# Kernel optimization log

Hardware: AMD Instinct MI355X
Metric: run time of the kernel (lower is better)

The kernel has to match this reference:

```python
import jax, jax.numpy as jnp
import numpy as np
from jax.experimental.ode import odeint

B, T, NV = 2048, 256, 32   # batch, time steps, n ICU variables
H, L, OH = 64, 32, 64      # gru hidden, latent dim, ode hidden


def setup_inputs() -> dict:
    key = jax.random.key(0)
    ks = jax.random.split(key, 24)
    def rn(k, shape, s):
        return (jax.random.normal(k, shape) * s).astype(jnp.float32)
    times = jnp.broadcast_to(jnp.linspace(0.0, 48.0, T, dtype=jnp.float32), (B, T))
    values = jax.random.normal(ks[0], (B, T, NV), dtype=jnp.float32)
    mask = (jax.random.uniform(ks[1], (B, T, NV)) < 0.5).astype(jnp.float32)
    seq_lengths = jnp.sort(jax.random.randint(ks[2], (B,), 1, T + 1))[::-1]
    seq_lengths = seq_lengths.at[0].set(T).astype(jnp.int32)
    eps = jax.random.normal(ks[3], (B, L), dtype=jnp.float32)
    return {
        "times": times, "values": values, "mask": mask,
        "seq_lengths": seq_lengths, "eps": eps,
        # GRU (torch layout: gates stacked r,z,n)
        "W_ih": rn(ks[4], (3 * H, 2 * NV), 0.1), "W_hh": rn(ks[5], (3 * H, H), 0.1),
        "b_ih": rn(ks[6], (3 * H,), 0.05), "b_hh": rn(ks[7], (3 * H,), 0.05),
        # hidden -> z0 params
        "W_z0": rn(ks[8], (2 * L, H), 0.1), "b_z0": rn(ks[9], (2 * L,), 0.05),
        # ODE func MLP (small weights keep dynamics tame for dopri5)
        "ode_W1": rn(ks[10], (OH, L), 0.05), "ode_b1": rn(ks[11], (OH,), 0.02),
        "ode_W2": rn(ks[12], (OH, OH), 0.05), "ode_b2": rn(ks[13], (OH,), 0.02),
        "ode_W3": rn(ks[14], (L, OH), 0.05), "ode_b3": rn(ks[15], (L,), 0.02),
        # decoder
        "dec_W1": rn(ks[16], (H, L), 0.1), "dec_b1": rn(ks[17], (H,), 0.05),
        "dec_W2": rn(ks[18], (1, H), 0.1), "dec_b2": rn(ks[19], (1,), 0.05),
    }


def _latent_ode_fwd(times, values, mask, seq_lengths, eps,
                    W_ih, W_hh, b_ih, b_hh, W_z0, b_z0,
                    ode_W1, ode_b1, ode_W2, ode_b2, ode_W3, ode_b3,
                    dec_W1, dec_b1, dec_W2, dec_b2):
    Bx, Tx = values.shape[0], values.shape[1]
    # encoder: concat (values, mask), flip time, run GRU over first seq_len steps
    x = jnp.concatenate([values, mask], axis=-1)[:, ::-1, :]          # [B,T,2NV]
    xp = jnp.einsum('btf,gf->tbg', x, W_ih) + b_ih                    # [T,B,3H]

    def gru_step(h, inp):
        xpt, t = inp                                                  # xpt: [B,3H]
        hh = h @ W_hh.T + b_hh
        xr, xz, xn = jnp.split(xpt, 3, axis=-1)
        hr, hz, hn = jnp.split(hh, 3, axis=-1)
        r = jax.nn.sigmoid(xr + hr)
        zg = jax.nn.sigmoid(xz + hz)
        n = jnp.tanh(xn + r * hn)
        h_new = (1.0 - zg) * n + zg * h
        h = jnp.where((t < seq_lengths)[:, None], h_new, h)           # packed-seq freeze
        return h, None

    h0 = jnp.zeros((Bx, W_hh.shape[1]), values.dtype)
    h, _ = jax.lax.scan(gru_step, h0, (xp, jnp.arange(Tx)))

    z0p = h @ W_z0.T + b_z0                                           # [B,2L]
    Ld = z0p.shape[-1] // 2
    z0_mean, z0_logvar = z0p[:, :Ld], z0p[:, Ld:]
    z0 = z0_mean + eps * jnp.exp(0.5 * z0_logvar)                     # reparameterize

    def ode_f(z, t, p):
        W1, b1, W2, b2, W3, b3 = p
        hl = jnp.tanh(z @ W1.T + b1)
        hl = jnp.tanh(hl @ W2.T + b2)
        return hl @ W3.T + b3

    t_span = jnp.array([0.0, 48.0], dtype=jnp.float32)
    traj = odeint(ode_f, z0, t_span,
                  (ode_W1, ode_b1, ode_W2, ode_b2, ode_W3, ode_b3),
                  rtol=1e-7, atol=1e-9)                               # dopri5, torchdiffeq defaults
    z_final = traj[-1]

    logits = (jax.nn.relu(z_final @ dec_W1.T + dec_b1) @ dec_W2.T + dec_b2)[:, 0]
    kl = -0.5 * jnp.mean(1.0 + z0_logvar - z0_mean ** 2 - jnp.exp(z0_logvar))
    return logits, kl


def reference(times, values, mask, seq_lengths, eps,
              W_ih, W_hh, b_ih, b_hh, W_z0, b_z0,
              ode_W1, ode_b1, ode_W2, ode_b2, ode_W3, ode_b3,
              dec_W1, dec_b1, dec_W2, dec_b2):
    return _latent_ode_fwd(times, values, mask, seq_lengths, eps,
                           W_ih, W_hh, b_ih, b_hh, W_z0, b_z0,
                           ode_W1, ode_b1, ode_W2, ode_b2, ode_W3, ode_b3,
                           dec_W1, dec_b1, dec_W2, dec_b2)
```

## Files before the change

### kernel.cpp

```cpp
#include <hip/hip_runtime.h>

#define B_ 2048
#define T_ 256
#define NV_ 32
#define H_ 64
#define L_ 32
#define OH_ 64
#define NSTEP 16
#define DEPTH 6

typedef _Float16 f16x8 __attribute__((ext_vector_type(8)));
typedef _Float16 f16x4 __attribute__((ext_vector_type(4)));
typedef float f32x4 __attribute__((ext_vector_type(4)));

#define MFMA16(a, b, c) __builtin_amdgcn_mfma_f32_16x16x32_f16((a), (b), (c), 0, 0, 0)

__device__ __forceinline__ float rcp_(float x) { return __builtin_amdgcn_rcpf(x); }
__device__ __forceinline__ float sigm(float x) { return rcp_(1.0f + __expf(-x)); }
__device__ __forceinline__ float tanh_(float x) { return 2.0f * rcp_(1.0f + __expf(-2.0f * x)) - 1.0f; }

__device__ __forceinline__ f16x8 pack8(f32x4 a, f32x4 b) {
    f16x8 r;
    r[0] = (_Float16)a[0]; r[1] = (_Float16)a[1]; r[2] = (_Float16)a[2]; r[3] = (_Float16)a[3];
    r[4] = (_Float16)b[0]; r[5] = (_Float16)b[1]; r[6] = (_Float16)b[2]; r[7] = (_Float16)b[3];
    return r;
}

__global__ __launch_bounds__(256) void gru_kernel(
    const float* __restrict__ values, const float* __restrict__ mask,
    const int* __restrict__ seql, const float* __restrict__ eps,
    const float* __restrict__ W_ih, const float* __restrict__ W_hh,
    const float* __restrict__ b_ih, const float* __restrict__ b_hh,
    const float* __restrict__ W_z0, const float* __restrict__ b_z0,
    float* __restrict__ z0ws, float* __restrict__ parts)
{
    const int tid = threadIdx.x;
    const int w   = tid >> 6;
    const int l   = tid & 63;
    const int c   = l & 15;
    const int g4  = l >> 4;
    const int b0  = blockIdx.x * 16;

    __shared__ unsigned h_u32[2][16][36];
    __shared__ float    zp_lds[16][68];
    __shared__ float    red_lds[4];
    __shared__ unsigned cnt;

    for (int i = tid; i < 2 * 16 * 36; i += 256) (&h_u32[0][0][0])[i] = 0u;
    if (tid == 0) cnt = 0u;

    f16x8 bih[3][2], bhh[3][2];
#pragma unroll
    for (int gate = 0; gate < 3; ++gate) {
#pragma unroll
        for (int kt = 0; kt < 2; ++kt) {
            const float* p1 = W_ih + (gate * 64 + w * 16 + c) * 64 + kt * 32 + g4 * 8;
            bih[gate][kt] = pack8(*(const f32x4*)p1, *(const f32x4*)(p1 + 4));
            const float* p2 = W_hh + (gate * 64 + w * 16 + c) * 64 + kt * 32 + g4 * 8;
            bhh[gate][kt] = pack8(*(const f32x4*)p2, *(const f32x4*)(p2 + 4));
        }
    }

    f32x4 bRq, bZq, bNXq, bNHq;
#pragma unroll
    for (int r = 0; r < 4; ++r) {
        const int f = w * 16 + g4 * 4 + r;
        bRq[r]  = b_ih[f]       + b_hh[f];
        bZq[r]  = b_ih[64 + f]  + b_hh[64 + f];
        bNXq[r] = b_ih[128 + f];
        bNHq[r] = b_hh[128 + f];
    }

    const int sl_c = seql[b0 + c];
    const int tmax = seql[b0];
    float hp[4] = {0.f, 0.f, 0.f, 0.f};

    const float* vrow = values + (size_t)(b0 + c) * T_ * NV_ + g4 * 8;
    const float* mrow = mask   + (size_t)(b0 + c) * T_ * NV_ + g4 * 8;

#define DECLSET(S) f32x4 S##v0, S##v1, S##m0, S##m1
    DECLSET(A); DECLSET(B); DECLSET(C); DECLSET(D); DECLSET(E); DECLSET(F);
#define FILLSET(S, tc) do {                                                  \
        const int tt_ = ((tc) < tmax) ? (tc) : 0;                            \
        const float* vp_ = vrow + (T_ - 1 - tt_) * NV_;                      \
        const float* mp_ = mrow + (T_ - 1 - tt_) * NV_;                      \
        S##v0 = *(const f32x4*)vp_; S##v1 = *(const f32x4*)(vp_ + 4);        \
        S##m0 = *(const f32x4*)mp_; S##m1 = *(const f32x4*)(mp_ + 4);        \
    } while (0)
    FILLSET(A, 0); FILLSET(B, 1); FILLSET(C, 2);
    FILLSET(D, 3); FILLSET(E, 4); FILLSET(F, 5);

    __syncthreads();

#define GSTEP(S, tc) do {                                                    \
        f16x8 ha0 = *(const f16x8*)&h_u32[(tc) & 1][c][4 * g4];              \
        f16x8 ha1 = *(const f16x8*)&h_u32[(tc) & 1][c][16 + 4 * g4];         \
        f16x8 xa0 = pack8(S##v0, S##v1);                                     \
        f16x8 xa1 = pack8(S##m0, S##m1);                                     \
        FILLSET(S, (tc) + DEPTH);                                            \
        f32x4 accR  = MFMA16(bih[0][0], xa0, bRq);                           \
        f32x4 accNX = MFMA16(bih[2][0], xa0, bNXq);                          \
        f32x4 accZ  = MFMA16(bih[1][0], xa0, bZq);                           \
        accR  = MFMA16(bih[0][1], xa1, accR);                                \
        accNX = MFMA16(bih[2][1], xa1, accNX);                               \
        accZ  = MFMA16(bih[1][1], xa1, accZ);                                \
        f32x4 accNH = MFMA16(bhh[2][0], ha0, bNHq);                          \
        accR  = MFMA16(bhh[0][0], ha0, accR);                                \
        accNH = MFMA16(bhh[2][1], ha1, accNH);                               \
        accR  = MFMA16(bhh[0][1], ha1, accR);                                \
        accZ  = MFMA16(bhh[1][0], ha0, accZ);                                \
        accZ  = MFMA16(bhh[1][1], ha1, accZ);                                \
        const bool act = ((tc) < sl_c);                                      \
        _Pragma("unroll")                                                    \
        for (int r = 0; r < 4; ++r) {                                        \
            float rr   = sigm(accR[r]);                                      \
            float zz   = sigm(accZ[r]);                                      \
            float nn   = tanh_(accNX[r] + rr * accNH[r]);                    \
            float hnew = nn + zz * (hp[r] - nn);                             \
            if (act) hp[r] = hnew;                                           \
        }                                                                    \
        f16x4 hq;                                                            \
        _Pragma("unroll")                                                    \
        for (int r = 0; r < 4; ++r) hq[r] = (_Float16)hp[r];                 \
        *(f16x4*)&h_u32[((tc) & 1) ^ 1][c][8 * w + 2 * g4] = hq;             \
        asm volatile("s_waitcnt lgkmcnt(0)" ::: "memory");                   \
        if (l == 0) atomicAdd(&cnt, 1u);                                     \
        asm volatile("" ::: "memory");                                       \
        {                                                                    \
            const unsigned tgt_ = 4u * ((unsigned)(tc) + 1u);                \
            while (__builtin_amdgcn_readfirstlane(                           \
                       *(volatile unsigned*)&cnt) < tgt_) { }                \
        }                                                                    \
        asm volatile("" ::: "memory");                                       \
    } while (0)

    int t = 0;
    while (true) {
        GSTEP(A, t); if (++t >= tmax) break;
        GSTEP(B, t); if (++t >= tmax) break;
        GSTEP(C, t); if (++t >= tmax) break;
        GSTEP(D, t); if (++t >= tmax) break;
        GSTEP(E, t); if (++t >= tmax) break;
        GSTEP(F, t); if (++t >= tmax) break;
    }

    f16x8 az0f[2];
#pragma unroll
    for (int kt = 0; kt < 2; ++kt) {
        const float* p = W_z0 + (w * 16 + c) * 64 + kt * 32 + g4 * 8;
        az0f[kt] = pack8(*(const f32x4*)p, *(const f32x4*)(p + 4));
    }
    const int fin = tmax & 1;
    f16x8 hf0 = *(const f16x8*)&h_u32[fin][c][4 * g4];
    f16x8 hf1 = *(const f16x8*)&h_u32[fin][c][16 + 4 * g4];
    f32x4 az;
#pragma unroll
    for (int r = 0; r < 4; ++r) az[r] = b_z0[w * 16 + g4 * 4 + r];
    az = MFMA16(az0f[0], hf0, az);
    az = MFMA16(az0f[1], hf1, az);
    *(f32x4*)&zp_lds[c][w * 16 + g4 * 4] = az;
    __syncthreads();

    const int row = tid >> 4;
    const int j2  = (tid & 15) * 2;
    float m0 = zp_lds[row][j2],      m1 = zp_lds[row][j2 + 1];
    float v0 = zp_lds[row][32 + j2], v1 = zp_lds[row][32 + j2 + 1];
    const float* erow = eps + (size_t)(b0 + row) * L_;
    float e0 = erow[j2], e1 = erow[j2 + 1];
    float* zrow = z0ws + (size_t)(b0 + row) * L_;
    float s0 = __expf(0.5f * v0), s1 = __expf(0.5f * v1);
    zrow[j2]     = m0 + e0 * s0;
    zrow[j2 + 1] = m1 + e1 * s1;
    float kls = (1.0f + v0 - m0 * m0 - s0 * s0) + (1.0f + v1 - m1 * m1 - s1 * s1);
#pragma unroll
    for (int off = 32; off >= 1; off >>= 1) kls += __shfl_down(kls, off);
    if (l == 0) red_lds[w] = kls;
    __syncthreads();
    if (tid == 0) parts[blockIdx.x] = red_lds[0] + red_lds[1] + red_lds[2] + red_lds[3];
}

__global__ __launch_bounds__(64) void ode_kernel(
    const float* __restrict__ z0ws,
    const float* __restrict__ oW1, const float* __restrict__ ob1,
    const float* __restrict__ oW2, const float* __restrict__ ob2,
    const float* __restrict__ oW3, const float* __restrict__ ob3,
    const float* __restrict__ dW1, const float* __restrict__ db1,
    const float* __restrict__ dW2, const float* __restrict__ db2,
    float* __restrict__ out)
{
    const int l  = threadIdx.x;
    const int c  = l & 15;
    const int g4 = l >> 4;
    const int b0 = blockIdx.x * 16;

    __shared__ _Float16 zbuf[16][40];
    __shared__ _Float16 buf1[16][72];
    __shared__ _Float16 buf2[16][72];

    f16x8 w1f[4], d1f[4], w2f[4][2], w3f[2][2];
#pragma unroll
    for (int mt = 0; mt < 4; ++mt) {
        const float* p = oW1 + (mt * 16 + c) * 32 + g4 * 8;
        w1f[mt] = pack8(*(const f32x4*)p, *(const f32x4*)(p + 4));
        const float* q = dW1 + (mt * 16 + c) * 32 + g4 * 8;
        d1f[mt] = pack8(*(const f32x4*)q, *(const f32x4*)(q + 4));
#pragma unroll
        for (int kt = 0; kt < 2; ++kt) {
            const float* r = oW2 + (mt * 16 + c) * 64 + kt * 32 + g4 * 8;
            w2f[mt][kt] = pack8(*(const f32x4*)r, *(const f32x4*)(r + 4));
        }
    }
#pragma unroll
    for (int mt = 0; mt < 2; ++mt) {
#pragma unroll
        for (int kt = 0; kt < 2; ++kt) {
            const float* r = oW3 + (mt * 16 + c) * 64 + kt * 32 + g4 * 8;
            w3f[mt][kt] = pack8(*(const f32x4*)r, *(const f32x4*)(r + 4));
        }
    }

    f32x4 b1q[4], b2q[4], d1q[4], w2q[4], b3q[2];
#pragma unroll
    for (int mt = 0; mt < 4; ++mt) {
#pragma unroll
        for (int r = 0; r < 4; ++r) {
            b1q[mt][r] = ob1[mt * 16 + g4 * 4 + r];
            b2q[mt][r] = ob2[mt * 16 + g4 * 4 + r];
            d1q[mt][r] = db1[mt * 16 + g4 * 4 + r];
            w2q[mt][r] = dW2[mt * 16 + g4 * 4 + r];
        }
    }
#pragma unroll
    for (int mt = 0; mt < 2; ++mt) {
#pragma unroll
        for (int r = 0; r < 4; ++r) b3q[mt][r] = ob3[mt * 16 + g4 * 4 + r];
    }
    const float bd2 = db2[0];

    f32x4 z[2];
#pragma unroll
    for (int mt = 0; mt < 2; ++mt)
        z[mt] = *(const f32x4*)(z0ws + (size_t)(b0 + c) * L_ + mt * 16 + g4 * 4);

    auto evalf = [&](const f32x4* zin, f32x4* kout) {
#pragma unroll
        for (int mt = 0; mt < 2; ++mt) {
            f16x4 hv;
#pragma unroll
            for (int r = 0; r < 4; ++r) hv[r] = (_Float16)zin[mt][r];
            *(f16x4*)&zbuf[c][mt * 16 + g4 * 4] = hv;
        }
        f16x8 zf = *(const f16x8*)&zbuf[c][g4 * 8];

        f32x4 h1[4];
#pragma unroll
        for (int mt = 0; mt < 4; ++mt) h1[mt] = MFMA16(w1f[mt], zf, b1q[mt]);
#pragma unroll
        for (int mt = 0; mt < 4; ++mt) {
            f16x4 hv;
#pragma unroll
            for (int r = 0; r < 4; ++r) hv[r] = (_Float16)tanh_(h1[mt][r]);
            *(f16x4*)&buf1[c][mt * 16 + g4 * 4] = hv;
        }
        f16x8 a1 = *(const f16x8*)&buf1[c][g4 * 8];
        f16x8 a2 = *(const f16x8*)&buf1[c][32 + g4 * 8];

        f32x4 h2[4];
#pragma unroll
        for (int mt = 0; mt < 4; ++mt) {
            h2[mt] = MFMA16(w2f[mt][0], a1, b2q[mt]);
            h2[mt] = MFMA16(w2f[mt][1], a2, h2[mt]);
        }
#pragma unroll
        for (int mt = 0; mt < 4; ++mt) {
            f16x4 hv;
#pragma unroll
            for (int r = 0; r < 4; ++r) hv[r] = (_Float16)tanh_(h2[mt][r]);
            *(f16x4*)&buf2[c][mt * 16 + g4 * 4] = hv;
        }
        f16x8 a3 = *(const f16x8*)&buf2[c][g4 * 8];
        f16x8 a4 = *(const f16x8*)&buf2[c][32 + g4 * 8];

#pragma unroll
        for (int mt = 0; mt < 2; ++mt) {
            kout[mt] = MFMA16(w3f[mt][0], a3, b3q[mt]);
            kout[mt] = MFMA16(w3f[mt][1], a4, kout[mt]);
        }
    };

    const float dt = 48.0f / (float)NSTEP;
    for (int s = 0; s < NSTEP; ++s) {
        f32x4 k[2], ks[2], zt[2];
        evalf(z, k);
#pragma unroll
        for (int mt = 0; mt < 2; ++mt) { ks[mt] = k[mt]; zt[mt] = z[mt] + k[mt] * (0.5f * dt); }
        evalf(zt, k);
#pragma unroll
        for (int mt = 0; mt < 2; ++mt) { ks[mt] += k[mt] * 2.0f; zt[mt] = z[mt] + k[mt] * (0.5f * dt); }
        evalf(zt, k);
#pragma unroll
        for (int mt = 0; mt < 2; ++mt) { ks[mt] += k[mt] * 2.0f; zt[mt] = z[mt] + k[mt] * dt; }
        evalf(zt, k);
#pragma unroll
        for (int mt = 0; mt < 2; ++mt) z[mt] += (ks[mt] + k[mt]) * (dt / 6.0f);
    }

#pragma unroll
    for (int mt = 0; mt < 2; ++mt) {
        f16x4 hv;
#pragma unroll
        for (int r = 0; r < 4; ++r) hv[r] = (_Float16)z[mt][r];
        *(f16x4*)&zbuf[c][mt * 16 + g4 * 4] = hv;
    }
    f16x8 zf = *(const f16x8*)&zbuf[c][g4 * 8];
    float p = 0.0f;
#pragma unroll
    for (int mt = 0; mt < 4; ++mt) {
        f32x4 d = MFMA16(d1f[mt], zf, d1q[mt]);
#pragma unroll
        for (int r = 0; r < 4; ++r) p += fmaxf(d[r], 0.0f) * w2q[mt][r];
    }
    p += __shfl_xor(p, 16);
    p += __shfl_xor(p, 32);
    if (l < 16) out[b0 + c] = p + bd2;
}

__global__ __launch_bounds__(128) void kl_fin(const float* __restrict__ parts,
                                              float* __restrict__ out)
{
    __shared__ float sred[2];
    const int tid = threadIdx.x;
    float p = parts[tid];
#pragma unroll
    for (int off = 32; off >= 1; off >>= 1) p += __shfl_down(p, off);
    if ((tid & 63) == 0) sred[tid >> 6] = p;
    __syncthreads();
    if (tid == 0) out[B_] = -0.5f * (sred[0] + sred[1]) / (float)(B_ * L_);
}

extern "C" void kernel_launch(void* const* d_in, const int* in_sizes, int n_in,
                              void* d_out, int out_size, void* d_ws, size_t ws_size,
                              hipStream_t stream) {
    const float* values = (const float*)d_in[1];
    const float* mask   = (const float*)d_in[2];
    const int*   seql   = (const int*)d_in[3];
    const float* eps    = (const float*)d_in[4];
    const float* W_ih   = (const float*)d_in[5];
    const float* W_hh   = (const float*)d_in[6];
    const float* b_ih   = (const float*)d_in[7];
    const float* b_hh   = (const float*)d_in[8];
    const float* W_z0   = (const float*)d_in[9];
    const float* b_z0   = (const float*)d_in[10];
    const float* oW1    = (const float*)d_in[11];
    const float* ob1    = (const float*)d_in[12];
    const float* oW2    = (const float*)d_in[13];
    const float* ob2    = (const float*)d_in[14];
    const float* oW3    = (const float*)d_in[15];
    const float* ob3    = (const float*)d_in[16];
    const float* dW1    = (const float*)d_in[17];
    const float* db1    = (const float*)d_in[18];
    const float* dW2    = (const float*)d_in[19];
    const float* db2    = (const float*)d_in[20];
    float* out = (float*)d_out;

    float* z0ws  = (float*)d_ws;
    float* parts = z0ws + (size_t)B_ * L_;

    hipLaunchKernelGGL(gru_kernel, dim3(B_ / 16), dim3(256), 0, stream,
                       values, mask, seql, eps, W_ih, W_hh, b_ih, b_hh, W_z0, b_z0,
                       z0ws, parts);
    hipLaunchKernelGGL(ode_kernel, dim3(B_ / 16), dim3(64), 0, stream,
                       z0ws, oW1, ob1, oW2, ob2, oW3, ob3, dW1, db1, dW2, db2, out);
    hipLaunchKernelGGL(kl_fin, dim3(1), dim3(128), 0, stream, parts, out);
}
```

Before: 225.5 us.

## Run each GRU batch tile in a single wave with hidden state in registers

The GRU kernel changes from four waves per 16-sample tile, which split the 64 hidden features and traded the hidden state through LDS with an atomic spin barrier every step, to one wave per tile that computes all four feature tiles itself. The hidden-unit order is permuted so the MFMA output layout lines up with the f16 B-operand layout, letting h be repacked from registers with no LDS round trip. This removes the per-step LDS exchange and cross-wave synchronization. In exchange each wave issues four times as many MFMAs per step, holds far more weight registers, and the grid has a quarter as many waves; the prefetch depth is also cut from 6 to 3 steps.

```diff
diff --git a/kernel.cpp b/kernel.cpp
--- a/kernel.cpp
+++ b/kernel.cpp
@@ -7,7 +7,7 @@
 #define L_ 32
 #define OH_ 64
 #define NSTEP 16
-#define DEPTH 6
+#define DEPTH 3
 
 typedef _Float16 f16x8 __attribute__((ext_vector_type(8)));
 typedef _Float16 f16x4 __attribute__((ext_vector_type(4)));
@@ -26,7 +26,7 @@
     return r;
 }
 
-__global__ __launch_bounds__(256) void gru_kernel(
+__global__ __launch_bounds__(64) void gru_kernel(
     const float* __restrict__ values, const float* __restrict__ mask,
     const int* __restrict__ seql, const float* __restrict__ eps,
     const float* __restrict__ W_ih, const float* __restrict__ W_hh,
@@ -34,52 +34,57 @@
     const float* __restrict__ W_z0, const float* __restrict__ b_z0,
     float* __restrict__ z0ws, float* __restrict__ parts)
 {
-    const int tid = threadIdx.x;
-    const int w   = tid >> 6;
-    const int l   = tid & 63;
-    const int c   = l & 15;
-    const int g4  = l >> 4;
-    const int b0  = blockIdx.x * 16;
-
-    __shared__ unsigned h_u32[2][16][36];
-    __shared__ float    zp_lds[16][68];
-    __shared__ float    red_lds[4];
-    __shared__ unsigned cnt;
-
-    for (int i = tid; i < 2 * 16 * 36; i += 256) (&h_u32[0][0][0])[i] = 0u;
-    if (tid == 0) cnt = 0u;
-
-    f16x8 bih[3][2], bhh[3][2];
-#pragma unroll
-    for (int gate = 0; gate < 3; ++gate) {
+    const int l  = threadIdx.x;
+    const int c  = l & 15;
+    const int g4 = l >> 4;
+    const int b0 = blockIdx.x * 16;
+
+    f16x8 wihR[4][2], wihZ[4][2], wihN[4][2];
+    f16x8 whhR[4][2], whhZ[4][2], whhN[4][2];
+#pragma unroll
+    for (int ft = 0; ft < 4; ++ft) {
+        const int sig = 8 * (c >> 2) + (c & 3) + 4 * (ft & 1) + 32 * (ft >> 1);
 #pragma unroll
         for (int kt = 0; kt < 2; ++kt) {
-            const float* p1 = W_ih + (gate * 64 + w * 16 + c) * 64 + kt * 32 + g4 * 8;
-            bih[gate][kt] = pack8(*(const f32x4*)p1, *(const f32x4*)(p1 + 4));
-            const float* p2 = W_hh + (gate * 64 + w * 16 + c) * 64 + kt * 32 + g4 * 8;
-            bhh[gate][kt] = pack8(*(const f32x4*)p2, *(const f32x4*)(p2 + 4));
-        }
-    }
-
-    f32x4 bRq, bZq, bNXq, bNHq;
-#pragma unroll
-    for (int r = 0; r < 4; ++r) {
-        const int f = w * 16 + g4 * 4 + r;
-        bRq[r]  = b_ih[f]       + b_hh[f];
-        bZq[r]  = b_ih[64 + f]  + b_hh[64 + f];
-        bNXq[r] = b_ih[128 + f];
-        bNHq[r] = b_hh[128 + f];
+            const float* pR = W_ih + (0 * 64 + sig) * 64 + kt * 32 + g4 * 8;
+            const float* pZ = W_ih + (1 * 64 + sig) * 64 + kt * 32 + g4 * 8;
+            const float* pN = W_ih + (2 * 64 + sig) * 64 + kt * 32 + g4 * 8;
+            wihR[ft][kt] = pack8(*(const f32x4*)pR, *(const f32x4*)(pR + 4));
+            wihZ[ft][kt] = pack8(*(const f32x4*)pZ, *(const f32x4*)(pZ + 4));
+            wihN[ft][kt] = pack8(*(const f32x4*)pN, *(const f32x4*)(pN + 4));
+            const float* qR = W_hh + (0 * 64 + sig) * 64 + kt * 32 + g4 * 8;
+            const float* qZ = W_hh + (1 * 64 + sig) * 64 + kt * 32 + g4 * 8;
+            const float* qN = W_hh + (2 * 64 + sig) * 64 + kt * 32 + g4 * 8;
+            whhR[ft][kt] = pack8(*(const f32x4*)qR, *(const f32x4*)(qR + 4));
+            whhZ[ft][kt] = pack8(*(const f32x4*)qZ, *(const f32x4*)(qZ + 4));
+            whhN[ft][kt] = pack8(*(const f32x4*)qN, *(const f32x4*)(qN + 4));
+        }
+    }
+
+    f32x4 bRq[4], bZq[4], bNXq[4], bNHq[4];
+#pragma unroll
+    for (int ft = 0; ft < 4; ++ft) {
+#pragma unroll
+        for (int r = 0; r < 4; ++r) {
+            const int fb = 8 * g4 + 4 * (ft & 1) + r + 32 * (ft >> 1);
+            bRq[ft][r]  = b_ih[fb]       + b_hh[fb];
+            bZq[ft][r]  = b_ih[64 + fb]  + b_hh[64 + fb];
+            bNXq[ft][r] = b_ih[128 + fb];
+            bNHq[ft][r] = b_hh[128 + fb];
+        }
     }
 
     const int sl_c = seql[b0 + c];
     const int tmax = seql[b0];
-    float hp[4] = {0.f, 0.f, 0.f, 0.f};
+
+    f32x4 hp4[4] = {{0.f,0.f,0.f,0.f},{0.f,0.f,0.f,0.f},
+                    {0.f,0.f,0.f,0.f},{0.f,0.f,0.f,0.f}};
 
     const float* vrow = values + (size_t)(b0 + c) * T_ * NV_ + g4 * 8;
     const float* mrow = mask   + (size_t)(b0 + c) * T_ * NV_ + g4 * 8;
 
 #define DECLSET(S) f32x4 S##v0, S##v1, S##m0, S##m1
-    DECLSET(A); DECLSET(B); DECLSET(C); DECLSET(D); DECLSET(E); DECLSET(F);
+    DECLSET(A); DECLSET(B); DECLSET(C);
 #define FILLSET(S, tc) do {                                                  \
         const int tt_ = ((tc) < tmax) ? (tc) : 0;                            \
         const float* vp_ = vrow + (T_ - 1 - tt_) * NV_;                      \
@@ -88,50 +93,41 @@
         S##m0 = *(const f32x4*)mp_; S##m1 = *(const f32x4*)(mp_ + 4);        \
     } while (0)
     FILLSET(A, 0); FILLSET(B, 1); FILLSET(C, 2);
-    FILLSET(D, 3); FILLSET(E, 4); FILLSET(F, 5);
-
-    __syncthreads();
 
 #define GSTEP(S, tc) do {                                                    \
-        f16x8 ha0 = *(const f16x8*)&h_u32[(tc) & 1][c][4 * g4];              \
-        f16x8 ha1 = *(const f16x8*)&h_u32[(tc) & 1][c][16 + 4 * g4];         \
         f16x8 xa0 = pack8(S##v0, S##v1);                                     \
         f16x8 xa1 = pack8(S##m0, S##m1);                                     \
         FILLSET(S, (tc) + DEPTH);                                            \
-        f32x4 accR  = MFMA16(bih[0][0], xa0, bRq);                           \
-        f32x4 accNX = MFMA16(bih[2][0], xa0, bNXq);                          \
-        f32x4 accZ  = MFMA16(bih[1][0], xa0, bZq);                           \
-        accR  = MFMA16(bih[0][1], xa1, accR);                                \
-        accNX = MFMA16(bih[2][1], xa1, accNX);                               \
-        accZ  = MFMA16(bih[1][1], xa1, accZ);                                \
-        f32x4 accNH = MFMA16(bhh[2][0], ha0, bNHq);                          \
-        accR  = MFMA16(bhh[0][0], ha0, accR);                                \
-        accNH = MFMA16(bhh[2][1], ha1, accNH);                               \
-        accR  = MFMA16(bhh[0][1], ha1, accR);                                \
-        accZ  = MFMA16(bhh[1][0], ha0, accZ);                                \
-        accZ  = MFMA16(bhh[1][1], ha1, accZ);                                \
+        f16x8 hb0 = pack8(hp4[0], hp4[1]);                                   \
+        f16x8 hb1 = pack8(hp4[2], hp4[3]);                                   \
+        f32x4 aR[4], aZ[4], aNX[4], aNH[4];                                  \
+        _Pragma("unroll")                                                    \
+        for (int ft = 0; ft < 4; ++ft) {                                     \
+            aR[ft]  = MFMA16(wihR[ft][0], xa0, bRq[ft]);                     \
+            aZ[ft]  = MFMA16(wihZ[ft][0], xa0, bZq[ft]);                     \
+            aNX[ft] = MFMA16(wihN[ft][0], xa0, bNXq[ft]);                    \
+            aR[ft]  = MFMA16(wihR[ft][1], xa1, aR[ft]);                      \
+            aZ[ft]  = MFMA16(wihZ[ft][1], xa1, aZ[ft]);                      \
+            aNX[ft] = MFMA16(wihN[ft][1], xa1, aNX[ft]);                     \
+            aNH[ft] = MFMA16(whhN[ft][0], hb0, bNHq[ft]);                    \
+            aR[ft]  = MFMA16(whhR[ft][0], hb0, aR[ft]);                      \
+            aZ[ft]  = MFMA16(whhZ[ft][0], hb0, aZ[ft]);                      \
+            aNH[ft] = MFMA16(whhN[ft][1], hb1, aNH[ft]);                     \
+            aR[ft]  = MFMA16(whhR[ft][1], hb1, aR[ft]);                      \
+            aZ[ft]  = MFMA16(whhZ[ft][1], hb1, aZ[ft]);                      \
+        }                                                                    \
         const bool act = ((tc) < sl_c);                                      \
         _Pragma("unroll")                                                    \
-        for (int r = 0; r < 4; ++r) {                                        \
-            float rr   = sigm(accR[r]);                                      \
-            float zz   = sigm(accZ[r]);                                      \
-            float nn   = tanh_(accNX[r] + rr * accNH[r]);                    \
-            float hnew = nn + zz * (hp[r] - nn);                             \
-            if (act) hp[r] = hnew;                                           \
+        for (int ft = 0; ft < 4; ++ft) {                                     \
+            _Pragma("unroll")                                                \
+            for (int r = 0; r < 4; ++r) {                                    \
+                float rr   = sigm(aR[ft][r]);                                \
+                float zz   = sigm(aZ[ft][r]);                                \
+                float nn   = tanh_(aNX[ft][r] + rr * aNH[ft][r]);            \
+                float hnew = nn + zz * (hp4[ft][r] - nn);                    \
+                if (act) hp4[ft][r] = hnew;                                  \
+            }                                                                \
         }                                                                    \
-        f16x4 hq;                                                            \
-        _Pragma("unroll")                                                    \
-        for (int r = 0; r < 4; ++r) hq[r] = (_Float16)hp[r];                 \
-        *(f16x4*)&h_u32[((tc) & 1) ^ 1][c][8 * w + 2 * g4] = hq;             \
-        asm volatile("s_waitcnt lgkmcnt(0)" ::: "memory");                   \
-        if (l == 0) atomicAdd(&cnt, 1u);                                     \
-        asm volatile("" ::: "memory");                                       \
-        {                                                                    \
-            const unsigned tgt_ = 4u * ((unsigned)(tc) + 1u);                \
-            while (__builtin_amdgcn_readfirstlane(                           \
-                       *(volatile unsigned*)&cnt) < tgt_) { }                \
-        }                                                                    \
-        asm volatile("" ::: "memory");                                       \
     } while (0)
 
     int t = 0;
@@ -139,44 +135,42 @@
         GSTEP(A, t); if (++t >= tmax) break;
         GSTEP(B, t); if (++t >= tmax) break;
         GSTEP(C, t); if (++t >= tmax) break;
-        GSTEP(D, t); if (++t >= tmax) break;
-        GSTEP(E, t); if (++t >= tmax) break;
-        GSTEP(F, t); if (++t >= tmax) break;
-    }
-
-    f16x8 az0f[2];
-#pragma unroll
-    for (int kt = 0; kt < 2; ++kt) {
-        const float* p = W_z0 + (w * 16 + c) * 64 + kt * 32 + g4 * 8;
-        az0f[kt] = pack8(*(const f32x4*)p, *(const f32x4*)(p + 4));
-    }
-    const int fin = tmax & 1;
-    f16x8 hf0 = *(const f16x8*)&h_u32[fin][c][4 * g4];
-    f16x8 hf1 = *(const f16x8*)&h_u32[fin][c][16 + 4 * g4];
-    f32x4 az;
-#pragma unroll
-    for (int r = 0; r < 4; ++r) az[r] = b_z0[w * 16 + g4 * 4 + r];
-    az = MFMA16(az0f[0], hf0, az);
-    az = MFMA16(az0f[1], hf1, az);
-    *(f32x4*)&zp_lds[c][w * 16 + g4 * 4] = az;
-    __syncthreads();
-
-    const int row = tid >> 4;
-    const int j2  = (tid & 15) * 2;
-    float m0 = zp_lds[row][j2],      m1 = zp_lds[row][j2 + 1];
-    float v0 = zp_lds[row][32 + j2], v1 = zp_lds[row][32 + j2 + 1];
-    const float* erow = eps + (size_t)(b0 + row) * L_;
-    float e0 = erow[j2], e1 = erow[j2 + 1];
-    float* zrow = z0ws + (size_t)(b0 + row) * L_;
-    float s0 = __expf(0.5f * v0), s1 = __expf(0.5f * v1);
-    zrow[j2]     = m0 + e0 * s0;
-    zrow[j2 + 1] = m1 + e1 * s1;
-    float kls = (1.0f + v0 - m0 * m0 - s0 * s0) + (1.0f + v1 - m1 * m1 - s1 * s1);
+    }
+
+    f16x8 hb0 = pack8(hp4[0], hp4[1]);
+    f16x8 hb1 = pack8(hp4[2], hp4[3]);
+    f32x4 az[4];
+#pragma unroll
+    for (int ft = 0; ft < 4; ++ft) {
+        f32x4 bz;
+#pragma unroll
+        for (int r = 0; r < 4; ++r) bz[r] = b_z0[ft * 16 + g4 * 4 + r];
+        const float* p0 = W_z0 + (ft * 16 + c) * 64 + g4 * 8;
+        const float* p1 = W_z0 + (ft * 16 + c) * 64 + 32 + g4 * 8;
+        f16x8 a0 = pack8(*(const f32x4*)p0, *(const f32x4*)(p0 + 4));
+        f16x8 a1 = pack8(*(const f32x4*)p1, *(const f32x4*)(p1 + 4));
+        az[ft] = MFMA16(a0, hb0, bz);
+        az[ft] = MFMA16(a1, hb1, az[ft]);
+    }
+    float kls = 0.0f;
+#pragma unroll
+    for (int pi = 0; pi < 2; ++pi) {
+        f32x4 m = az[pi];
+        f32x4 v = az[pi + 2];
+        const int j0 = pi * 16 + g4 * 4;
+        f32x4 e = *(const f32x4*)(eps + (size_t)(b0 + c) * L_ + j0);
+        f32x4 zo;
+#pragma unroll
+        for (int r = 0; r < 4; ++r) {
+            float s = __expf(0.5f * v[r]);
+            zo[r] = m[r] + e[r] * s;
+            kls += 1.0f + v[r] - m[r] * m[r] - s * s;
+        }
+        *(f32x4*)(z0ws + (size_t)(b0 + c) * L_ + j0) = zo;
+    }
 #pragma unroll
     for (int off = 32; off >= 1; off >>= 1) kls += __shfl_down(kls, off);
-    if (l == 0) red_lds[w] = kls;
-    __syncthreads();
-    if (tid == 0) parts[blockIdx.x] = red_lds[0] + red_lds[1] + red_lds[2] + red_lds[3];
+    if (l == 0) parts[blockIdx.x] = kls;
 }
 
 __global__ __launch_bounds__(64) void ode_kernel(
@@ -366,7 +360,7 @@
     float* z0ws  = (float*)d_ws;
     float* parts = z0ws + (size_t)B_ * L_;
 
-    hipLaunchKernelGGL(gru_kernel, dim3(B_ / 16), dim3(256), 0, stream,
+    hipLaunchKernelGGL(gru_kernel, dim3(B_ / 16), dim3(64), 0, stream,
                        values, mask, seql, eps, W_ih, W_hh, b_ih, b_hh, W_z0, b_z0,
                        z0ws, parts);
     hipLaunchKernelGGL(ode_kernel, dim3(B_ / 16), dim3(64), 0, stream,
```

New measurement: 444.8 us. 1.97x slower.
